# Performance work log

Hardware: AMD Instinct MI355X
Metric: run time of the kernel (lower is better)

Reference implementation:

```python
import jax, jax.numpy as jnp
import numpy as np

EPS = 1e-8
LRELU_SLOPE = 0.2


def leaky_relu(x, p=LRELU_SLOPE):
    return jnp.where(x >= 0, x, p * x)


def conv2dmod(x, weight, style):
    """StyleGAN2 weight-demodulated conv.
    x: [B,C_in,H,W], weight: [C_out,C_in,k,k], style: [B,C_in]."""
    # per-sample modulation: scale input channels by (style + 1)
    w = weight[None] * (style[:, None, :, None, None] + 1.0)  # [B,O,I,k,k]
    # demodulation: rescale each output filter to unit norm
    d = jax.lax.rsqrt(jnp.sum(w * w, axis=(2, 3, 4), keepdims=True) + EPS)
    w = w * d

    def conv_one(xi, wi):
        # xi: [C_in,H,W], wi: [O,I,k,k] -> [O,H,W]
        return jax.lax.conv_general_dilated(
            xi[None], wi, window_strides=(1, 1), padding='SAME',
            dimension_numbers=('NCHW', 'OIHW', 'NCHW'))[0]

    return jax.vmap(conv_one)(x, w)  # [B,O,H,W]


def setup_inputs() -> dict:
    key = jax.random.key(0)
    ks = jax.random.split(key, 9)
    B, C_in, C_out, H, W = 16, 128, 256, 128, 128
    return {
        "features": jax.random.normal(ks[0], (B, C_in, H, W), jnp.float32),
        "style_mean1": jax.random.normal(ks[1], (B, C_in, 1, 1), jnp.float32),
        "style_std1": jax.random.normal(ks[2], (B, C_in, 1, 1), jnp.float32),
        "style_mean2": jax.random.normal(ks[3], (B, C_in, 1, 1), jnp.float32),
        "style_std2": jax.random.normal(ks[4], (B, C_in, 1, 1), jnp.float32),
        "lastBlockBool": 0,
        "w1": jax.random.normal(ks[5], (C_in, C_in, 3, 3), jnp.float32),
        "w2": jax.random.normal(ks[6], (C_in, C_in, 3, 3), jnp.float32),
        "down_w": jax.random.normal(ks[7], (C_out, C_in, 4, 4), jnp.float32) * 0.05,
        "down_b": jnp.zeros((C_out,), jnp.float32),
    }


def reference(features, style_mean1, style_std1, style_mean2, style_std2,
              lastBlockBool, w1, w2, down_w, down_b):
    # style_mean2/style_std2/lastBlockBool are accepted but unused by the
    # original forward; dropout is identity (eval mode).
    s1 = style_mean1[:, :, 0, 0]  # squeeze(-1).squeeze(-1) -> [B,C_in]
    s2 = style_std1[:, :, 0, 0]
    x = leaky_relu(conv2dmod(features, w1, s1))
    x = leaky_relu(conv2dmod(x, w2, s2) + x)  # residual
    # downsample: 4x4 conv, stride 2, pad 1 -> halves H,W
    y = jax.lax.conv_general_dilated(
        x, down_w, window_strides=(2, 2), padding=((1, 1), (1, 1)),
        dimension_numbers=('NCHW', 'OIHW', 'NCHW'))
    return y + down_b[None, :, None, None]
```

## Files before the change

kernel.cpp:

```cpp
#include <hip/hip_runtime.h>
#include <hip/hip_bf16.h>

constexpr int B  = 16;
constexpr int C  = 128;
constexpr int H  = 128;
constexpr int W  = 128;
constexpr int CO = 256;
constexpr int HO = 64;
constexpr int WO = 64;

#define EPSV   1e-8f
#define SLOPE  0.2f

typedef short bf16x8 __attribute__((ext_vector_type(8)));
typedef float f32x4  __attribute__((ext_vector_type(4)));

typedef const __attribute__((address_space(1))) unsigned int  gbl_u32;
typedef __attribute__((address_space(3))) unsigned int        lds_u32;

__device__ __forceinline__ void bar_raw() {
    asm volatile("" ::: "memory");
    __builtin_amdgcn_s_barrier();
    asm volatile("" ::: "memory");
}
#define WAITV(N) asm volatile("s_waitcnt vmcnt(" #N ")" ::: "memory")

__device__ __forceinline__ short f2bs(float v) {
    __hip_bfloat16 h = __float2bfloat16(v);
    return *(short*)&h;
}
__device__ __forceinline__ float bs2f(short s) {
    __hip_bfloat16 h = *(__hip_bfloat16*)&s;
    return __bfloat162float(h);
}

__global__ __launch_bounds__(128) void demod_kernel(
    const float* __restrict__ w1, const float* __restrict__ w2,
    const float* __restrict__ s1, const float* __restrict__ s2,
    float* __restrict__ d)
{
    int bid  = blockIdx.x;
    int conv = bid >> 11;
    int b    = (bid >> 7) & 15;
    int o    = bid & 127;
    const float* w = conv ? w2 : w1;
    const float* s = conv ? s2 : s1;
    int i = threadIdx.x;
    float sv = s[b * C + i] + 1.0f;
    const float* wp = w + (o * C + i) * 9;
    float sum = 0.f;
    #pragma unroll
    for (int k = 0; k < 9; ++k) { float t = wp[k] * sv; sum += t * t; }
    #pragma unroll
    for (int off = 32; off; off >>= 1) sum += __shfl_down(sum, off);
    __shared__ float red[2];
    if ((threadIdx.x & 63) == 0) red[threadIdx.x >> 6] = sum;
    __syncthreads();
    if (threadIdx.x == 0) d[bid] = rsqrtf(red[0] + red[1] + EPSV);
}

__global__ __launch_bounds__(256) void expand_kernel(
    const float* __restrict__ w1, const float* __restrict__ w2,
    const float* __restrict__ s1, const float* __restrict__ s2,
    const float* __restrict__ d, short* __restrict__ wm)
{
    int idx = blockIdx.x * 256 + threadIdx.x;
    int ic  = idx & 127;
    int oc  = (idx >> 7) & 127;
    int t   = idx >> 14;
    int tap = t % 9;
    int cb  = t / 9;
    int b   = cb & 15;
    int conv= cb >> 4;
    const float* w = conv ? w2 : w1;
    const float* s = conv ? s2 : s1;
    float v = w[(oc * C + ic) * 9 + tap] * (s[b * C + ic] + 1.0f)
            * d[(conv * B + b) * C + oc];
    int icH = ic >> 6, icL = (ic >> 5) & 1;
    int dst = cb * 147456
            + ((icH * 18 + tap * 2 + icL) * 8 + (oc >> 4)) * 512
            + ((ic >> 3) & 3) * 128 + (oc & 15) * 8 + (ic & 7);
    wm[dst] = f2bs(v);
}

__global__ __launch_bounds__(256) void dwexpand_kernel(
    const float* __restrict__ dw, short* __restrict__ dwm)
{
    int idx = blockIdx.x * 256 + threadIdx.x;
    int ic  = idx & 127;
    int oc  = (idx >> 7) & 255;
    int tap = idx >> 15;
    int dst = ((ic >> 5) * 16 + tap) * 8192 + (oc >> 4) * 512
            + ((ic >> 3) & 3) * 128 + (oc & 15) * 8 + (ic & 7);
    dwm[dst] = f2bs(dw[(oc * C + ic) * 16 + tap]);
}

__global__ __launch_bounds__(256) void nchw2nhwc_kernel(
    const float* __restrict__ in, short* __restrict__ out)
{
    __shared__ short s[128 * 136];
    int bid = blockIdx.x;
    int h = bid & 127, b = bid >> 7;
    int tid = threadIdx.x;
    for (int i = tid; i < 128 * 32; i += 256) {
        int w4 = i & 31, ic = i >> 5;
        float4 v = *(const float4*)&in[((b * C + ic) * H + h) * W + w4 * 4];
        s[(w4 * 4 + 0) * 136 + ic] = f2bs(v.x);
        s[(w4 * 4 + 1) * 136 + ic] = f2bs(v.y);
        s[(w4 * 4 + 2) * 136 + ic] = f2bs(v.z);
        s[(w4 * 4 + 3) * 136 + ic] = f2bs(v.w);
    }
    __syncthreads();
    for (int i = tid; i < 128 * 16; i += 256) {
        int icg = i & 15, w = i >> 4;
        *(uint4*)&out[((b * H + h) * W + w) * C + icg * 8] =
            *(uint4*)&s[w * 136 + icg * 8];
    }
}

__global__ __launch_bounds__(256, 4) void conv3x3_mfma(
    const short* __restrict__ in, const short* __restrict__ wmc,
    const short* __restrict__ res, short* __restrict__ out)
{
    __shared__ short sIn[180 * 64];
    __shared__ short sW[2][4096];

    int bid = blockIdx.x;
    int wt = bid & 7, ht = (bid >> 3) & 15, b = bid >> 7;
    int w0 = wt * 16, h0 = ht * 8;
    int tid  = threadIdx.x;
    int lane = tid & 63, wv = tid >> 6;
    int q = lane >> 4, l15 = lane & 15;
    int wr = wv & 1;
    int wc = wv >> 1;

    const short* wb = wmc + b * 147456;

    auto stageIn = [&](int st) {
        for (int i = tid; i < 180 * 8; i += 256) {
            int slot = i & 7, pix = i >> 3;
            int hl = pix / 18, wl = pix - hl * 18;
            int gh = h0 - 1 + hl, gw = w0 - 1 + wl;
            uint4 v = make_uint4(0u, 0u, 0u, 0u);
            if ((unsigned)gh < (unsigned)H && (unsigned)gw < (unsigned)W)
                v = *(const uint4*)&in[((b * H + gh) * W + gw) * C + st * 64 + slot * 8];
            *(uint4*)&sIn[pix * 64 + ((slot ^ (pix & 7)) << 3)] = v;
        }
    };
    auto stageW = [&](int st, int s, int buf) {
        #pragma unroll
        for (int i = 0; i < 2; ++i) {
            const short* g = wb + st * 73728 + s * 4096
                           + (wv * 2 + i) * 512 + lane * 8;
            __builtin_amdgcn_global_load_lds(
                (gbl_u32*)g, (lds_u32*)&sW[buf][(wv * 2 + i) * 512], 16, 0, 0);
        }
    };

    f32x4 acc[4][4];
    #pragma unroll
    for (int mt = 0; mt < 4; ++mt)
        #pragma unroll
        for (int nt = 0; nt < 4; ++nt)
            acc[mt][nt] = (f32x4){0.f, 0.f, 0.f, 0.f};

    stageW(0, 0, 0);
    stageIn(0);
    __syncthreads();

    int bfbase = q * 128 + l15 * 8;

    #pragma unroll 1
    for (int st = 0; st < 2; ++st) {
        #pragma unroll 2
        for (int s = 0; s < 18; ++s) {
            int tap = s >> 1, icL = s & 1;
            int dh = tap / 3, dwd = tap - dh * 3;
            if (s < 17)        stageW(st, s + 1, (s + 1) & 1);
            else if (st == 0)  stageW(1, 0, 0);
            if (st == 1 && s == 17) { WAITV(0); } else { WAITV(2); }
            bar_raw();
            bf16x8 af[4], bf[4];
            #pragma unroll
            for (int mt = 0; mt < 4; ++mt) {
                int pix  = (wr * 4 + mt + dh) * 18 + l15 + dwd;
                int slot = (icL * 4 + q) ^ (pix & 7);
                af[mt] = *(const bf16x8*)&sIn[pix * 64 + slot * 8];
            }
            #pragma unroll
            for (int nt = 0; nt < 4; ++nt)
                bf[nt] = *(const bf16x8*)&sW[s & 1][(wc * 4 + nt) * 512 + bfbase];
            #pragma unroll
            for (int mt = 0; mt < 4; ++mt)
                #pragma unroll
                for (int nt = 0; nt < 4; ++nt)
                    acc[mt][nt] = __builtin_amdgcn_mfma_f32_16x16x32_bf16(
                        af[mt], bf[nt], acc[mt][nt], 0, 0, 0);
            bar_raw();
        }
        if (st == 0) { stageIn(1); __syncthreads(); }
    }

    bool has_res = (res != nullptr);
    #pragma unroll
    for (int mt = 0; mt < 4; ++mt) {
        int h = h0 + wr * 4 + mt;
        #pragma unroll
        for (int nt = 0; nt < 4; ++nt) {
            int oc = wc * 64 + nt * 16 + l15;
            #pragma unroll
            for (int reg = 0; reg < 4; ++reg) {
                int w = w0 + q * 4 + reg;
                int idx = ((b * H + h) * W + w) * C + oc;
                float v = acc[mt][nt][reg];
                if (has_res) v += bs2f(res[idx]);
                v = v >= 0.f ? v : SLOPE * v;
                out[idx] = f2bs(v);
            }
        }
    }
}

__global__ __launch_bounds__(256, 2) void downconv_mfma(
    const short* __restrict__ in, const short* __restrict__ dwm,
    const float* __restrict__ db, float* __restrict__ out)
{
    __shared__ short sIn[2 * 306 * 32];
    __shared__ short sW[2][8192];

    int bid = blockIdx.x;
    int wt = bid & 3;
    int ht = (bid >> 2) & 7;
    int b  = bid >> 5;
    int ow0 = wt * 16, oh0 = ht * 8;
    int ih0 = 2 * oh0 - 1, iw0 = 2 * ow0 - 1;

    int tid  = threadIdx.x;
    int lane = tid & 63, wv = tid >> 6;
    int q = lane >> 4, l15 = lane & 15;

    auto stageIn = [&](int icC) {
        for (int i = tid; i < 612 * 4; i += 256) {
            int slot = i & 3, pix = i >> 2;
            int ihl = pix / 34, iwl = pix - ihl * 34;
            int gh = ih0 + ihl, gw = iw0 + iwl;
            uint4 v = make_uint4(0u, 0u, 0u, 0u);
            if ((unsigned)gh < (unsigned)H && (unsigned)gw < (unsigned)W)
                v = *(const uint4*)&in[((b * H + gh) * W + gw) * C + icC * 32 + slot * 8];
            int par = iwl & 1, pl = ihl * 17 + (iwl >> 1);
            *(uint4*)&sIn[(par * 306 + pl) * 32 + ((slot ^ ((pl >> 1) & 3)) << 3)] = v;
        }
    };
    auto stageW = [&](int s) {
        #pragma unroll
        for (int j = 0; j < 4; ++j) {
            int base = (j * 4 + wv) * 512;
            const short* g = dwm + s * 8192 + base + lane * 8;
            __builtin_amdgcn_global_load_lds(
                (gbl_u32*)g, (lds_u32*)&sW[s & 1][base], 16, 0, 0);
        }
    };

    f32x4 acc[4][8];
    #pragma unroll
    for (int mt = 0; mt < 4; ++mt)
        #pragma unroll
        for (int nt = 0; nt < 8; ++nt)
            acc[mt][nt] = (f32x4){0.f, 0.f, 0.f, 0.f};

    stageW(0);
    stageIn(0);
    __syncthreads();

    const int abase = q * 128 + l15 * 8;

    #pragma unroll 1
    for (int icC = 0; icC < 4; ++icC) {
        #pragma unroll 2
        for (int tap = 0; tap < 16; ++tap) {
            int step = icC * 16 + tap;
            if (step < 63) stageW(step + 1);
            if (step < 63) { WAITV(4); } else { WAITV(0); }
            bar_raw();
            const int dh = tap >> 2, dwn = tap & 3;
            const int par = dwn & 1, cb0 = dwn >> 1;
            bf16x8 af[4], bf[8];
            #pragma unroll
            for (int mt = 0; mt < 4; ++mt)
                af[mt] = *(const bf16x8*)&sW[tap & 1][(wv * 4 + mt) * 512 + abase];
            #pragma unroll
            for (int nt = 0; nt < 8; ++nt) {
                int pl = (2 * nt + dh) * 17 + cb0 + l15;
                bf[nt] = *(const bf16x8*)&sIn[(par * 306 + pl) * 32
                                              + ((q ^ ((pl >> 1) & 3)) << 3)];
            }
            #pragma unroll
            for (int mt = 0; mt < 4; ++mt)
                #pragma unroll
                for (int nt = 0; nt < 8; ++nt)
                    acc[mt][nt] = __builtin_amdgcn_mfma_f32_16x16x32_bf16(
                        af[mt], bf[nt], acc[mt][nt], 0, 0, 0);
            bar_raw();
        }
        if (icC < 3) { stageIn(icC + 1); __syncthreads(); }
    }

    #pragma unroll
    for (int mt = 0; mt < 4; ++mt) {
        f32x4 bi = *(const f32x4*)&db[(wv * 4 + mt) * 16 + q * 4];
        #pragma unroll
        for (int nt = 0; nt < 8; ++nt) {
            int oh = oh0 + nt;
            #pragma unroll
            for (int reg = 0; reg < 4; ++reg) {
                int oc = (wv * 4 + mt) * 16 + q * 4 + reg;
                out[((b * CO + oc) * HO + oh) * WO + ow0 + l15] =
                    acc[mt][nt][reg] + bi[reg];
            }
        }
    }
}

extern "C" void kernel_launch(void* const* d_in, const int* in_sizes, int n_in,
                              void* d_out, int out_size, void* d_ws, size_t ws_size,
                              hipStream_t stream) {
    const float* features = (const float*)d_in[0];
    const float* sm1      = (const float*)d_in[1];
    const float* ss1      = (const float*)d_in[2];
    const float* w1       = (const float*)d_in[6];
    const float* w2       = (const float*)d_in[7];
    const float* dw       = (const float*)d_in[8];
    const float* db       = (const float*)d_in[9];
    float* out = (float*)d_out;

    char* ws = (char*)d_ws;
    short* x1  = (short*)ws;
    short* x2  = (short*)(ws + 67108864);
    short* wm  = (short*)(ws + 134217728);
    short* dwm = (short*)(ws + 143654912);
    float* dv  = (float*)(ws + 144703488);

    demod_kernel    <<<4096, 128, 0, stream>>>(w1, w2, sm1, ss1, dv);
    expand_kernel   <<<18432, 256, 0, stream>>>(w1, w2, sm1, ss1, dv, wm);
    dwexpand_kernel <<<2048, 256, 0, stream>>>(dw, dwm);
    nchw2nhwc_kernel<<<2048, 256, 0, stream>>>(features, x2);
    conv3x3_mfma    <<<2048, 256, 0, stream>>>(x2, wm, nullptr, x1);
    conv3x3_mfma    <<<2048, 256, 0, stream>>>(x1, wm + 16 * 147456, x1, x2);
    downconv_mfma   <<<512, 256, 0, stream>>>(x2, dwm, db, out);
}
```

Baseline: 317.5 us.

## Triple-buffer conv3x3 weight stages and pad input LDS tile instead of swizzle

Moves the 3x3 MFMA conv's weight staging from double to triple buffering, prefetching two stages ahead. This drops one of the two barriers per step and flattens the two-stage loop into a fully unrolled 36-step loop. The input tile's XOR swizzle is replaced by padding rows to 72 elements, which simplifies the A-fragment address math into constant offsets. The cost is more LDS, and launch bounds are lowered to 3 blocks per SM, so occupancy may drop and register pressure from full unrolling may rise.

```diff
diff --git a/kernel.cpp b/kernel.cpp
--- a/kernel.cpp
+++ b/kernel.cpp
@@ -118,12 +118,12 @@
     }
 }
 
-__global__ __launch_bounds__(256, 4) void conv3x3_mfma(
+__global__ __launch_bounds__(256, 3) void conv3x3_mfma(
     const short* __restrict__ in, const short* __restrict__ wmc,
     const short* __restrict__ res, short* __restrict__ out)
 {
-    __shared__ short sIn[180 * 64];
-    __shared__ short sW[2][4096];
+    __shared__ short sW[3][4096];
+    __shared__ short sIn[180 * 72];
 
     int bid = blockIdx.x;
     int wt = bid & 7, ht = (bid >> 3) & 15, b = bid >> 7;
@@ -144,16 +144,16 @@
             uint4 v = make_uint4(0u, 0u, 0u, 0u);
             if ((unsigned)gh < (unsigned)H && (unsigned)gw < (unsigned)W)
                 v = *(const uint4*)&in[((b * H + gh) * W + gw) * C + st * 64 + slot * 8];
-            *(uint4*)&sIn[pix * 64 + ((slot ^ (pix & 7)) << 3)] = v;
+            *(uint4*)&sIn[pix * 72 + slot * 8] = v;
         }
     };
-    auto stageW = [&](int st, int s, int buf) {
+    auto stageW = [&](int s) {
         #pragma unroll
         for (int i = 0; i < 2; ++i) {
-            const short* g = wb + st * 73728 + s * 4096
+            const short* g = wb + (s / 18) * 73728 + (s % 18) * 4096
                            + (wv * 2 + i) * 512 + lane * 8;
             __builtin_amdgcn_global_load_lds(
-                (gbl_u32*)g, (lds_u32*)&sW[buf][(wv * 2 + i) * 512], 16, 0, 0);
+                (gbl_u32*)g, (lds_u32*)&sW[s % 3][(wv * 2 + i) * 512], 16, 0, 0);
         }
     };
 
@@ -164,41 +164,39 @@
         for (int nt = 0; nt < 4; ++nt)
             acc[mt][nt] = (f32x4){0.f, 0.f, 0.f, 0.f};
 
-    stageW(0, 0, 0);
-    stageIn(0);
+    stageW(0); stageW(1); stageIn(0);
     __syncthreads();
 
-    int bfbase = q * 128 + l15 * 8;
-
-    #pragma unroll 1
-    for (int st = 0; st < 2; ++st) {
-        #pragma unroll 2
-        for (int s = 0; s < 18; ++s) {
-            int tap = s >> 1, icL = s & 1;
-            int dh = tap / 3, dwd = tap - dh * 3;
-            if (s < 17)        stageW(st, s + 1, (s + 1) & 1);
-            else if (st == 0)  stageW(1, 0, 0);
-            if (st == 1 && s == 17) { WAITV(0); } else { WAITV(2); }
+    const int abase = ((wr * 4) * 18 + l15) * 72 + q * 8;
+    const int bbase = q * 128 + l15 * 8;
+
+    #pragma unroll
+    for (int s = 0; s < 36; ++s) {
+        if (s == 18) {
             bar_raw();
-            bf16x8 af[4], bf[4];
-            #pragma unroll
-            for (int mt = 0; mt < 4; ++mt) {
-                int pix  = (wr * 4 + mt + dh) * 18 + l15 + dwd;
-                int slot = (icL * 4 + q) ^ (pix & 7);
-                af[mt] = *(const bf16x8*)&sIn[pix * 64 + slot * 8];
-            }
+            stageIn(1);
+            __syncthreads();
+        } else {
+            if (s == 35) { WAITV(0); } else { WAITV(2); }
+            bar_raw();
+        }
+        if (s + 2 < 36) stageW(s + 2);
+        const int loc = s % 18, tap = loc >> 1, icL = loc & 1;
+        const int dh = tap / 3, dwd = tap - dh * 3;
+        bf16x8 af[4], bf[4];
+        #pragma unroll
+        for (int mt = 0; mt < 4; ++mt)
+            af[mt] = *(const bf16x8*)&sIn[abase + ((mt + dh) * 18 + dwd) * 72
+                                          + icL * 32];
+        #pragma unroll
+        for (int nt = 0; nt < 4; ++nt)
+            bf[nt] = *(const bf16x8*)&sW[s % 3][(wc * 4 + nt) * 512 + bbase];
+        #pragma unroll
+        for (int mt = 0; mt < 4; ++mt)
             #pragma unroll
             for (int nt = 0; nt < 4; ++nt)
-                bf[nt] = *(const bf16x8*)&sW[s & 1][(wc * 4 + nt) * 512 + bfbase];
-            #pragma unroll
-            for (int mt = 0; mt < 4; ++mt)
-                #pragma unroll
-                for (int nt = 0; nt < 4; ++nt)
-                    acc[mt][nt] = __builtin_amdgcn_mfma_f32_16x16x32_bf16(
-                        af[mt], bf[nt], acc[mt][nt], 0, 0, 0);
-            bar_raw();
-        }
-        if (st == 0) { stageIn(1); __syncthreads(); }
+                acc[mt][nt] = __builtin_amdgcn_mfma_f32_16x16x32_bf16(
+                    af[mt], bf[nt], acc[mt][nt], 0, 0, 0);
     }
 
     bool has_res = (res != nullptr);
```

Measured after the change: 331.0 us. 1.04x slower.

## Split conv3x3 input-channel staging into four 32-channel chunks to cut LDS

Applied to the files above, without the earlier changes.

Restructures the 3x3 modulated conv loop to stage the input halo tile in four 32-channel chunks instead of two 64-channel chunks. This halves the sIn LDS footprint and raises launch bounds to 5 blocks per CU. Weight staging is reindexed per (chunk, tap), and the swizzle changes to a 4-slot XOR. The cost is more stageIn phases with full __syncthreads stalls, during which no weight-load/compute overlap happens.

```diff
diff --git a/kernel.cpp b/kernel.cpp
--- a/kernel.cpp
+++ b/kernel.cpp
@@ -118,11 +118,11 @@
     }
 }
 
-__global__ __launch_bounds__(256, 4) void conv3x3_mfma(
+__global__ __launch_bounds__(256, 5) void conv3x3_mfma(
     const short* __restrict__ in, const short* __restrict__ wmc,
     const short* __restrict__ res, short* __restrict__ out)
 {
-    __shared__ short sIn[180 * 64];
+    __shared__ short sIn[180 * 32];
     __shared__ short sW[2][4096];
 
     int bid = blockIdx.x;
@@ -136,21 +136,22 @@
 
     const short* wb = wmc + b * 147456;
 
-    auto stageIn = [&](int st) {
-        for (int i = tid; i < 180 * 8; i += 256) {
-            int slot = i & 7, pix = i >> 3;
+    auto stageIn = [&](int icC) {
+        for (int i = tid; i < 180 * 4; i += 256) {
+            int slot = i & 3, pix = i >> 2;
             int hl = pix / 18, wl = pix - hl * 18;
             int gh = h0 - 1 + hl, gw = w0 - 1 + wl;
             uint4 v = make_uint4(0u, 0u, 0u, 0u);
             if ((unsigned)gh < (unsigned)H && (unsigned)gw < (unsigned)W)
-                v = *(const uint4*)&in[((b * H + gh) * W + gw) * C + st * 64 + slot * 8];
-            *(uint4*)&sIn[pix * 64 + ((slot ^ (pix & 7)) << 3)] = v;
+                v = *(const uint4*)&in[((b * H + gh) * W + gw) * C + icC * 32 + slot * 8];
+            *(uint4*)&sIn[pix * 32 + ((slot ^ (pix & 3)) << 3)] = v;
         }
     };
-    auto stageW = [&](int st, int s, int buf) {
+    auto stageW = [&](int stg, int tap, int buf) {
+        int icH = stg >> 1, icL = stg & 1;
         #pragma unroll
         for (int i = 0; i < 2; ++i) {
-            const short* g = wb + st * 73728 + s * 4096
+            const short* g = wb + icH * 73728 + (tap * 2 + icL) * 4096
                            + (wv * 2 + i) * 512 + lane * 8;
             __builtin_amdgcn_global_load_lds(
                 (gbl_u32*)g, (lds_u32*)&sW[buf][(wv * 2 + i) * 512], 16, 0, 0);
@@ -168,28 +169,28 @@
     stageIn(0);
     __syncthreads();
 
-    int bfbase = q * 128 + l15 * 8;
+    const int bbase = q * 128 + l15 * 8;
 
     #pragma unroll 1
-    for (int st = 0; st < 2; ++st) {
-        #pragma unroll 2
-        for (int s = 0; s < 18; ++s) {
-            int tap = s >> 1, icL = s & 1;
-            int dh = tap / 3, dwd = tap - dh * 3;
-            if (s < 17)        stageW(st, s + 1, (s + 1) & 1);
-            else if (st == 0)  stageW(1, 0, 0);
-            if (st == 1 && s == 17) { WAITV(0); } else { WAITV(2); }
+    for (int stg = 0; stg < 4; ++stg) {
+        #pragma unroll 3
+        for (int tap = 0; tap < 9; ++tap) {
+            int g = stg * 9 + tap;
+            if (tap < 8)       stageW(stg, tap + 1, (g + 1) & 1);
+            else if (stg < 3)  stageW(stg + 1, 0, (g + 1) & 1);
+            if (stg == 3 && tap == 8) { WAITV(0); } else { WAITV(2); }
             bar_raw();
+            const int dh = tap / 3, dwd = tap - dh * 3;
             bf16x8 af[4], bf[4];
             #pragma unroll
             for (int mt = 0; mt < 4; ++mt) {
                 int pix  = (wr * 4 + mt + dh) * 18 + l15 + dwd;
-                int slot = (icL * 4 + q) ^ (pix & 7);
-                af[mt] = *(const bf16x8*)&sIn[pix * 64 + slot * 8];
+                int slot = q ^ (pix & 3);
+                af[mt] = *(const bf16x8*)&sIn[pix * 32 + slot * 8];
             }
             #pragma unroll
             for (int nt = 0; nt < 4; ++nt)
-                bf[nt] = *(const bf16x8*)&sW[s & 1][(wc * 4 + nt) * 512 + bfbase];
+                bf[nt] = *(const bf16x8*)&sW[g & 1][(wc * 4 + nt) * 512 + bbase];
             #pragma unroll
             for (int mt = 0; mt < 4; ++mt)
                 #pragma unroll
@@ -198,7 +199,7 @@
                         af[mt], bf[nt], acc[mt][nt], 0, 0, 0);
             bar_raw();
         }
-        if (st == 0) { stageIn(1); __syncthreads(); }
+        if (stg < 3) { stageIn(stg + 1); __syncthreads(); }
     }
 
     bool has_res = (res != nullptr);
```

Result: slower. 765.5 us (+141.1%).
